# Kernel tuning notes

Hardware: AMD Instinct MI355X
Metric: run time of the kernel (lower is better)

Reference implementation:

```python
import jax, jax.numpy as jnp
import numpy as np

N = 100000
E = 1600000
IN_C = 128
HID = 128
OUT_C = 2
EPS = 1e-5


def gcn_conv(x, src, dst, norm, W, b, num_nodes):
    # PyG GCNConv: linear transform then symmetric-normalized scatter-add
    h = x @ W                                  # [N, out]
    msg = h[src] * norm[:, None]               # [E+N, out] gather
    out = jax.ops.segment_sum(msg, dst, num_segments=num_nodes)
    return out + b


def batchnorm_eval(x, gamma, beta, rm, rv):
    inv = gamma / jnp.sqrt(rv + EPS)
    return (x - rm) * inv + beta


def setup_inputs() -> dict:
    key = jax.random.key(0)
    ks = jax.random.split(key, 16)
    x = jax.random.normal(ks[0], (N, IN_C), dtype=jnp.float32)
    edge_index = jax.random.randint(ks[1], (2, E), 0, N, dtype=jnp.int32)
    s = 1.0 / np.sqrt(IN_C)
    W1 = jax.random.uniform(ks[2], (IN_C, HID), jnp.float32, -s, s)
    b1 = jnp.zeros((HID,), jnp.float32)
    g1 = jnp.ones((HID,), jnp.float32)
    be1 = jnp.zeros((HID,), jnp.float32)
    rm1 = jax.random.normal(ks[3], (HID,), jnp.float32) * 0.1
    rv1 = jax.random.uniform(ks[4], (HID,), jnp.float32, 0.5, 1.5)
    s2 = 1.0 / np.sqrt(HID)
    W2 = jax.random.uniform(ks[5], (HID, HID), jnp.float32, -s2, s2)
    b2 = jnp.zeros((HID,), jnp.float32)
    g2 = jnp.ones((HID,), jnp.float32)
    be2 = jnp.zeros((HID,), jnp.float32)
    rm2 = jax.random.normal(ks[6], (HID,), jnp.float32) * 0.1
    rv2 = jax.random.uniform(ks[7], (HID,), jnp.float32, 0.5, 1.5)
    W3 = jax.random.uniform(ks[8], (HID, OUT_C), jnp.float32, -s2, s2)
    b3 = jnp.zeros((OUT_C,), jnp.float32)
    return {"x": x, "edge_index": edge_index,
            "W1": W1, "b1": b1, "g1": g1, "be1": be1, "rm1": rm1, "rv1": rv1,
            "W2": W2, "b2": b2, "g2": g2, "be2": be2, "rm2": rm2, "rv2": rv2,
            "W3": W3, "b3": b3}


def reference(x, edge_index, W1, b1, g1, be1, rm1, rv1,
              W2, b2, g2, be2, rm2, rv2, W3, b3):
    num_nodes = x.shape[0]
    loops = jnp.arange(num_nodes, dtype=edge_index.dtype)
    src = jnp.concatenate([edge_index[0], loops])   # add self loops
    dst = jnp.concatenate([edge_index[1], loops])
    deg = jax.ops.segment_sum(jnp.ones_like(dst, dtype=x.dtype), dst,
                              num_segments=num_nodes)
    dinv = jax.lax.rsqrt(deg)                        # deg >= 1 with self loops
    norm = dinv[src] * dinv[dst]                     # [E+N]

    h = gcn_conv(x, src, dst, norm, W1, b1, num_nodes)
    h = jax.nn.relu(batchnorm_eval(h, g1, be1, rm1, rv1))
    h = gcn_conv(h, src, dst, norm, W2, b2, num_nodes)
    h = jax.nn.relu(batchnorm_eval(h, g2, be2, rm2, rv2))
    out = gcn_conv(h, src, dst, norm, W3, b3, num_nodes)
    return out
```

## Files before the change

kernel.cpp:

```cpp
#include <hip/hip_runtime.h>

#define NN 100000
#define EE 1600000
#define CH 128

typedef _Float16 h2 __attribute__((ext_vector_type(2)));
typedef _Float16 h8 __attribute__((ext_vector_type(8)));
typedef float f32x4 __attribute__((ext_vector_type(4)));

#define S_NODES 512
#define NBUCK 196
#define CAP_E 10240

#define CHUNK_STRIDE ((size_t)NN * 16)


__global__ __launch_bounds__(256) void k_passA(const int* __restrict__ src, const int* __restrict__ dst,
                                               int* __restrict__ gcur, int* __restrict__ eb) {
    __shared__ int hist[NBUCK];
    __shared__ int curL[NBUCK];
    for (int t = threadIdx.x; t < NBUCK; t += 256) hist[t] = 0;
    __syncthreads();
    int base = blockIdx.x * 4096;
    int pk[16], bk[16];
#pragma unroll
    for (int j = 0; j < 16; ++j) {
        int i = base + threadIdx.x + 256 * j;
        if (i < EE) {
            int s = src[i], d = dst[i];
            bk[j] = d >> 9;
            pk[j] = (s << 9) | (d & 511);
            atomicAdd(&hist[bk[j]], 1);
        } else bk[j] = -1;
    }
    __syncthreads();
    for (int t = threadIdx.x; t < NBUCK; t += 256) {
        int h = hist[t];
        curL[t] = (h > 0) ? atomicAdd(&gcur[t], h) : 0;
    }
    __syncthreads();
#pragma unroll
    for (int j = 0; j < 16; ++j) {
        if (bk[j] >= 0) {
            int pos = atomicAdd(&curL[bk[j]], 1);
            if (pos < CAP_E) eb[bk[j] * CAP_E + pos] = pk[j];
        }
    }
}


__global__ __launch_bounds__(256) void k_bscan(const int* __restrict__ gcur, int* __restrict__ bbase,
                                               int* __restrict__ rp) {
    __shared__ int ts[256];
    int t = threadIdx.x;
    int nn = (t < NBUCK) ? min(S_NODES, NN - t * S_NODES) : 0;
    int v = (t < NBUCK) ? (min(gcur[t], CAP_E) + nn) : 0;
    ts[t] = v; __syncthreads();
    for (int off = 1; off < 256; off <<= 1) {
        int u = (t >= off) ? ts[t - off] : 0;
        __syncthreads();
        ts[t] += u;
        __syncthreads();
    }
    if (t < NBUCK) bbase[t] = ts[t] - v;
    if (t == 0) rp[NN] = EE + NN;
}


__global__ __launch_bounds__(256) void k_passB(const int* __restrict__ gcur, const int* __restrict__ eb,
                                               const int* __restrict__ bbase, int* __restrict__ rp,
                                               float* __restrict__ dinv, int* __restrict__ col) {
    __shared__ int c[S_NODES];
    __shared__ int excl[S_NODES];
    __shared__ int cur[S_NODES];
    __shared__ int ts[256];
    __shared__ int stage[CAP_E + S_NODES];
    int bId = blockIdx.x;
    int nbase = bId * S_NODES;
    int tid = threadIdx.x;
    c[tid] = 0; c[tid + 256] = 0;
    __syncthreads();
    int n = min(gcur[bId], CAP_E);
    const int* e = eb + (size_t)bId * CAP_E;
    for (int i = tid; i < n; i += 256) atomicAdd(&c[e[i] & 511], 1);
    __syncthreads();
    int n0 = nbase + 2 * tid, n1 = n0 + 1;
    int v0 = (n0 < NN) ? c[2 * tid] + 1 : 0;
    int v1 = (n1 < NN) ? c[2 * tid + 1] + 1 : 0;
    int s = v0 + v1;
    ts[tid] = s; __syncthreads();
    for (int off = 1; off < 256; off <<= 1) {
        int u = (tid >= off) ? ts[tid - off] : 0;
        __syncthreads();
        ts[tid] += u;
        __syncthreads();
    }
    int ex = ts[tid] - s;
    int base = bbase[bId];
    excl[2 * tid] = ex; excl[2 * tid + 1] = ex + v0;
    cur[2 * tid] = ex;  cur[2 * tid + 1] = ex + v0;
    if (n0 < NN) { rp[n0] = base + ex;      dinv[n0] = rsqrtf((float)v0); }
    if (n1 < NN) { rp[n1] = base + ex + v0; dinv[n1] = rsqrtf((float)v1); }
    __syncthreads();
    for (int i = tid; i < n; i += 256) {
        int pe = e[i];
        int pos = atomicAdd(&cur[pe & 511], 1);
        stage[pos] = pe >> 9;
    }
    {
        int t0 = 2 * tid, t1 = 2 * tid + 1;
        if (n0 < NN) stage[excl[t0] + c[t0]] = n0;
        if (n1 < NN) stage[excl[t1] + c[t1]] = n1;
    }
    __syncthreads();
    int total = ts[255];
    for (int i = tid; i < total; i += 256) col[base + i] = stage[i];
}


__global__ __launch_bounds__(128) void k_prep(const float* __restrict__ W1, const float* __restrict__ W2,
                                              _Float16* __restrict__ Wt1, _Float16* __restrict__ Wt2,
                                              const float* __restrict__ b1, const float* __restrict__ g1,
                                              const float* __restrict__ be1, const float* __restrict__ rm1,
                                              const float* __restrict__ rv1,
                                              const float* __restrict__ b2, const float* __restrict__ g2,
                                              const float* __restrict__ be2, const float* __restrict__ rm2,
                                              const float* __restrict__ rv2,
                                              float* __restrict__ sc1, float* __restrict__ sh1,
                                              float* __restrict__ sc2, float* __restrict__ sh2) {
    int bid = blockIdx.x, t = threadIdx.x;
    if (bid < 128) {
        Wt1[bid * 128 + t] = (_Float16)W1[t * 128 + bid];
    } else if (bid < 256) {
        int nn = bid - 128;
        Wt2[nn * 128 + t] = (_Float16)W2[t * 128 + nn];
    } else if (bid == 256) {
        float sv = g1[t] * rsqrtf(rv1[t] + 1e-5f);
        sc1[t] = sv;
        sh1[t] = (b1[t] - rm1[t]) * sv + be1[t];
    } else {
        float sv = g2[t] * rsqrtf(rv2[t] + 1e-5f);
        sc2[t] = sv;
        sh2[t] = (b2[t] - rm2[t]) * sv + be2[t];
    }
}


template <bool F32IN>
__global__ __launch_bounds__(256) void k_gemm_mfma(const void* __restrict__ Ain,
                                                   const _Float16* __restrict__ Wt,
                                                   const float* __restrict__ dinv,
                                                   _Float16* __restrict__ C) {
    __shared__ _Float16 Wl[CH * CH];
    {
        const float4* wg = (const float4*)Wt;
#pragma unroll
        for (int i = 0; i < 8; ++i) {
            int chunk = i * 256 + threadIdx.x;
            int row = chunk >> 4, slot = chunk & 15;
            float4 v = wg[chunk];
            *(float4*)((char*)Wl + row * 256 + ((slot ^ (row & 15)) * 16)) = v;
        }
    }
    __syncthreads();
    int lane = threadIdx.x & 63;
    int l15 = lane & 15, lhi = lane >> 4;
    int row0 = blockIdx.x * 64 + (threadIdx.x >> 6) * 16;
    if (row0 >= NN) return;

    h8 afrag[4];
    if (F32IN) {
        const float* Arow = (const float*)Ain + (size_t)(row0 + l15) * CH + lhi * 8;
#pragma unroll
        for (int ks = 0; ks < 4; ++ks) {
            float4 a = *(const float4*)(Arow + ks * 32);
            float4 b = *(const float4*)(Arow + ks * 32 + 4);
            h8 o;
            o[0] = (_Float16)a.x; o[1] = (_Float16)a.y; o[2] = (_Float16)a.z; o[3] = (_Float16)a.w;
            o[4] = (_Float16)b.x; o[5] = (_Float16)b.y; o[6] = (_Float16)b.z; o[7] = (_Float16)b.w;
            afrag[ks] = o;
        }
    } else {
        const _Float16* Ah = (const _Float16*)Ain;
#pragma unroll
        for (int ks = 0; ks < 4; ++ks) {
            int chunk = ks * 2 + (lhi >> 1);
            afrag[ks] = *(const h8*)(Ah + (size_t)chunk * CHUNK_STRIDE
                                     + (size_t)(row0 + l15) * 16 + (lhi & 1) * 8);
        }
    }

    f32x4 acc[8] = {};
#pragma unroll
    for (int ks = 0; ks < 4; ++ks) {
        int slot = ks * 4 + lhi;
#pragma unroll
        for (int c = 0; c < 8; ++c) {
            int brow = c * 16 + l15;
            h8 b = *(const h8*)((char*)Wl + brow * 256 + ((slot ^ (brow & 15)) * 16));
            acc[c] = __builtin_amdgcn_mfma_f32_16x16x32_f16(afrag[ks], b, acc[c], 0, 0, 0);
        }
    }
    float dv[4];
#pragma unroll
    for (int j = 0; j < 4; ++j) dv[j] = dinv[row0 + lhi * 4 + j];
#pragma unroll
    for (int c = 0; c < 8; ++c)
#pragma unroll
        for (int j = 0; j < 4; ++j) {
            float v = acc[c][j] * dv[j];
            C[(size_t)c * CHUNK_STRIDE + (size_t)(row0 + lhi * 4 + j) * 16 + l15] = (_Float16)v;
        }
}


__global__ __launch_bounds__(256) void k_aggs3(const _Float16* __restrict__ h, const int* __restrict__ rp,
                                               const int* __restrict__ col, const float* __restrict__ dinv,
                                               const float* __restrict__ sc, const float* __restrict__ sh,
                                               _Float16* __restrict__ out) {
    int s = blockIdx.x & 7;
    int gb = blockIdx.x >> 3;
    int lane = threadIdx.x & 63;
    int g = lane >> 3;
    int c = lane & 7;
    int node = gb * 32 + (threadIdx.x >> 6) * 8 + g;
    int beg = rp[node];
    int end = rp[node + 1];
    int md = end - beg;
    md = max(md, __shfl_xor(md, 8));
    md = max(md, __shfl_xor(md, 16));
    md = max(md, __shfl_xor(md, 32));
    const _Float16* hs = h + (size_t)s * CHUNK_STRIDE;
    float ax = 0.f, ay = 0.f, bx = 0.f, by = 0.f;
    for (int e = 0; e < md; e += 8) {
        int sv[8]; float m[8];
#pragma unroll
        for (int j = 0; j < 8; ++j) {
            int i = beg + e + j;
            m[j] = (i < end) ? 1.f : 0.f;
            sv[j] = col[i < end ? i : beg];
        }
        h2 v[8];
#pragma unroll
        for (int j = 0; j < 8; ++j)
            v[j] = *(const h2*)(hs + ((size_t)sv[j] << 4) + c * 2);
#pragma unroll
        for (int j = 0; j < 8; j += 2) {
            ax = fmaf((float)v[j][0],     m[j],     ax);
            ay = fmaf((float)v[j][1],     m[j],     ay);
            bx = fmaf((float)v[j + 1][0], m[j + 1], bx);
            by = fmaf((float)v[j + 1][1], m[j + 1], by);
        }
    }
    ax += bx; ay += by;
    float dvn = dinv[node];
    float2 scv = *(const float2*)(sc + s * 16 + c * 2);
    float2 shv = *(const float2*)(sh + s * 16 + c * 2);
    float o0 = fmaxf(fmaf(ax * dvn, scv.x, shv.x), 0.f);
    float o1 = fmaxf(fmaf(ay * dvn, scv.y, shv.y), 0.f);
    h2 o; o[0] = (_Float16)o0; o[1] = (_Float16)o1;
    *(h2*)(out + (size_t)s * CHUNK_STRIDE + (size_t)node * 16 + c * 2) = o;
}


__global__ __launch_bounds__(256) void k_gemm_out(const _Float16* __restrict__ A, const float* __restrict__ W3,
                                                  const float* __restrict__ dinv, float* __restrict__ H3) {
    __shared__ float w3s[256];
    w3s[threadIdx.x] = W3[threadIdx.x];
    __syncthreads();
    int n = blockIdx.x * 256 + threadIdx.x;
    if (n >= NN) return;
    float a0 = 0.f, a1 = 0.f;
#pragma unroll
    for (int c = 0; c < 8; ++c) {
        h8 a = *(const h8*)(A + (size_t)c * CHUNK_STRIDE + (size_t)n * 16);
        h8 b = *(const h8*)(A + (size_t)c * CHUNK_STRIDE + (size_t)n * 16 + 8);
#pragma unroll
        for (int j = 0; j < 8; ++j) {
            int k = c * 16 + j;
            a0 += (float)a[j] * w3s[k * 2];
            a1 += (float)a[j] * w3s[k * 2 + 1];
        }
#pragma unroll
        for (int j = 0; j < 8; ++j) {
            int k = c * 16 + 8 + j;
            a0 += (float)b[j] * w3s[k * 2];
            a1 += (float)b[j] * w3s[k * 2 + 1];
        }
    }
    float dv = dinv[n];
    *(float2*)(H3 + (size_t)n * 2) = make_float2(a0 * dv, a1 * dv);
}

__global__ __launch_bounds__(256) void k_agg_out(const float* __restrict__ H3, const int* __restrict__ rp,
                                                 const int* __restrict__ col, const float* __restrict__ dinv,
                                                 const float* __restrict__ b3, float* __restrict__ out) {
    int n = blockIdx.x * 256 + threadIdx.x;
    if (n >= NN) return;
    int beg = rp[n], end = rp[n + 1];
    float a0 = 0.f, a1 = 0.f;
    for (int e = beg; e < end; ++e) {
        int s = col[e];
        float2 hv = *(const float2*)(H3 + (size_t)s * 2);
        a0 += hv.x;
        a1 += hv.y;
    }
    float dv = dinv[n];
    out[(size_t)n * 2 + 0] = fmaf(a0, dv, b3[0]);
    out[(size_t)n * 2 + 1] = fmaf(a1, dv, b3[1]);
}


extern "C" void kernel_launch(void* const* d_in, const int* in_sizes, int n_in,
                              void* d_out, int out_size, void* d_ws, size_t ws_size,
                              hipStream_t stream) {
    const float* x  = (const float*)d_in[0];
    const int* ei   = (const int*)d_in[1];
    const int* src  = ei;
    const int* dst  = ei + EE;
    const float* W1 = (const float*)d_in[2];
    const float* b1 = (const float*)d_in[3];
    const float* g1 = (const float*)d_in[4];
    const float* be1 = (const float*)d_in[5];
    const float* rm1 = (const float*)d_in[6];
    const float* rv1 = (const float*)d_in[7];
    const float* W2 = (const float*)d_in[8];
    const float* b2 = (const float*)d_in[9];
    const float* g2 = (const float*)d_in[10];
    const float* be2 = (const float*)d_in[11];
    const float* rm2 = (const float*)d_in[12];
    const float* rv2 = (const float*)d_in[13];
    const float* W3 = (const float*)d_in[14];
    const float* b3 = (const float*)d_in[15];
    float* out = (float*)d_out;

    char* p = (char*)d_ws;
    auto carve = [&](size_t bytes) -> void* {
        void* r = (void*)p;
        p += (bytes + 255) & ~(size_t)255;
        return r;
    };
    int* rp     = (int*)carve((size_t)(NN + 1) * 4);
    float* dinv = (float*)carve((size_t)NN * 4);
    int* col    = (int*)carve((size_t)(EE + NN) * 4);
    int* bbase  = (int*)carve(256 * 4);
    float* sc1  = (float*)carve(128 * 4);
    float* sh1  = (float*)carve(128 * 4);
    float* sc2  = (float*)carve(128 * 4);
    float* sh2  = (float*)carve(128 * 4);
    _Float16* bufA = (_Float16*)carve((size_t)NN * CH * 2);
    _Float16* bufB = (_Float16*)carve((size_t)NN * CH * 2);
    _Float16* Wt1  = (_Float16*)carve(128 * 128 * 2);
    _Float16* Wt2  = (_Float16*)carve(128 * 128 * 2);
    float* h3   = (float*)carve((size_t)NN * 2 * 4);

    int* eb   = (int*)bufA;
    int* gcur = eb + (size_t)NBUCK * CAP_E;

    hipMemsetAsync(gcur, 0, (size_t)NBUCK * 4, stream);

    k_passA<<<(EE + 4095) / 4096, 256, 0, stream>>>(src, dst, gcur, eb);
    k_bscan<<<1, 256, 0, stream>>>(gcur, bbase, rp);
    k_passB<<<NBUCK, 256, 0, stream>>>(gcur, eb, bbase, rp, dinv, col);
    k_prep<<<258, 128, 0, stream>>>(W1, W2, Wt1, Wt2,
                                    b1, g1, be1, rm1, rv1,
                                    b2, g2, be2, rm2, rv2,
                                    sc1, sh1, sc2, sh2);

    int aggBlocks = 8 * (NN / 32);
    k_gemm_mfma<true><<<(NN + 63) / 64, 256, 0, stream>>>(x, Wt1, dinv, bufA);
    k_aggs3<<<aggBlocks, 256, 0, stream>>>(bufA, rp, col, dinv, sc1, sh1, bufB);
    k_gemm_mfma<false><<<(NN + 63) / 64, 256, 0, stream>>>(bufB, Wt2, dinv, bufA);
    k_aggs3<<<aggBlocks, 256, 0, stream>>>(bufA, rp, col, dinv, sc2, sh2, bufB);
    k_gemm_out<<<(NN + 255) / 256, 256, 0, stream>>>(bufB, W3, dinv, h3);
    k_agg_out<<<(NN + 255) / 256, 256, 0, stream>>>(h3, rp, col, dinv, b3, out);
}
```

Baseline: 270.0 us.

## Sort nodes by degree and aggregate 32 nodes per wave with 16-byte gathers

Adds a counting sort of nodes by in-degree (histogram, scan, scatter into a permutation), so each wavefront in the hidden-layer aggregation handles 32 nodes of similar degree. The per-wave loop bound, which is the maximum degree in the wave, then stays close to every node's own degree. Each lane now gathers 8 halves (16 bytes) per edge instead of 2, which cuts the number of load instructions. The cost is three extra small kernels, two extra memsets and some padding on the col array, and neighbouring output rows are no longer written together.

```diff
diff --git a/kernel.cpp b/kernel.cpp
--- a/kernel.cpp
+++ b/kernel.cpp
@@ -69,7 +69,8 @@
 
 __global__ __launch_bounds__(256) void k_passB(const int* __restrict__ gcur, const int* __restrict__ eb,
                                                const int* __restrict__ bbase, int* __restrict__ rp,
-                                               float* __restrict__ dinv, int* __restrict__ col) {
+                                               float* __restrict__ dinv, int* __restrict__ col,
+                                               int* __restrict__ deg) {
     __shared__ int c[S_NODES];
     __shared__ int excl[S_NODES];
     __shared__ int cur[S_NODES];
@@ -99,8 +100,8 @@
     int base = bbase[bId];
     excl[2 * tid] = ex; excl[2 * tid + 1] = ex + v0;
     cur[2 * tid] = ex;  cur[2 * tid + 1] = ex + v0;
-    if (n0 < NN) { rp[n0] = base + ex;      dinv[n0] = rsqrtf((float)v0); }
-    if (n1 < NN) { rp[n1] = base + ex + v0; dinv[n1] = rsqrtf((float)v1); }
+    if (n0 < NN) { rp[n0] = base + ex;      dinv[n0] = rsqrtf((float)v0); deg[n0] = v0; }
+    if (n1 < NN) { rp[n1] = base + ex + v0; dinv[n1] = rsqrtf((float)v1); deg[n1] = v1; }
     __syncthreads();
     for (int i = tid; i < n; i += 256) {
         int pe = e[i];
@@ -115,6 +116,51 @@
     __syncthreads();
     int total = ts[255];
     for (int i = tid; i < total; i += 256) col[base + i] = stage[i];
+}
+
+
+__global__ __launch_bounds__(256) void k_dhist(const int* __restrict__ deg, int* __restrict__ ghist) {
+    __shared__ int lh[64];
+    int tid = threadIdx.x;
+    if (tid < 64) lh[tid] = 0;
+    __syncthreads();
+    int node = blockIdx.x * 256 + tid;
+    if (node < NN) atomicAdd(&lh[min(deg[node], 63)], 1);
+    __syncthreads();
+    if (tid < 64 && lh[tid] > 0) atomicAdd(&ghist[tid], lh[tid]);
+}
+
+__global__ __launch_bounds__(64) void k_dscan(const int* __restrict__ ghist, int* __restrict__ gcur) {
+    __shared__ int ts[64];
+    int t = threadIdx.x;
+    int v = ghist[t];
+    ts[t] = v; __syncthreads();
+    for (int off = 1; off < 64; off <<= 1) {
+        int u = (t >= off) ? ts[t - off] : 0;
+        __syncthreads();
+        ts[t] += u;
+        __syncthreads();
+    }
+    gcur[t] = ts[t] - v;
+}
+
+__global__ __launch_bounds__(256) void k_dsort(const int* __restrict__ deg, int* __restrict__ gcur,
+                                               int* __restrict__ perm) {
+    __shared__ int lh[64];
+    __shared__ int lbase[64];
+    int tid = threadIdx.x;
+    if (tid < 64) lh[tid] = 0;
+    __syncthreads();
+    int node = blockIdx.x * 256 + tid;
+    int d = -1, lr = 0;
+    if (node < NN) {
+        d = min(deg[node], 63);
+        lr = atomicAdd(&lh[d], 1);
+    }
+    __syncthreads();
+    if (tid < 64) lbase[tid] = (lh[tid] > 0) ? atomicAdd(&gcur[tid], lh[tid]) : 0;
+    __syncthreads();
+    if (node < NN) perm[lbase[d] + lr] = node;
 }
 
 
@@ -214,52 +260,63 @@
 }
 
 
-__global__ __launch_bounds__(256) void k_aggs3(const _Float16* __restrict__ h, const int* __restrict__ rp,
-                                               const int* __restrict__ col, const float* __restrict__ dinv,
+#define UNROLL 8
+
+__global__ __launch_bounds__(256) void k_aggs4(const _Float16* __restrict__ h, const int* __restrict__ rp,
+                                               const int* __restrict__ col, const int* __restrict__ perm,
+                                               const float* __restrict__ dinv,
                                                const float* __restrict__ sc, const float* __restrict__ sh,
                                                _Float16* __restrict__ out) {
     int s = blockIdx.x & 7;
-    int gb = blockIdx.x >> 3;
+    int gw = (blockIdx.x >> 3) * 4 + (threadIdx.x >> 6);
+    int base = gw * 32;
+    if (base >= NN) return;
     int lane = threadIdx.x & 63;
-    int g = lane >> 3;
-    int c = lane & 7;
-    int node = gb * 32 + (threadIdx.x >> 6) * 8 + g;
-    int beg = rp[node];
-    int end = rp[node + 1];
+    int half = lane & 1;
+    int node = perm[base + (lane >> 1)];
+    int beg = rp[node], end = rp[node + 1];
     int md = end - beg;
+    md = max(md, __shfl_xor(md, 2));
+    md = max(md, __shfl_xor(md, 4));
     md = max(md, __shfl_xor(md, 8));
     md = max(md, __shfl_xor(md, 16));
     md = max(md, __shfl_xor(md, 32));
-    const _Float16* hs = h + (size_t)s * CHUNK_STRIDE;
-    float ax = 0.f, ay = 0.f, bx = 0.f, by = 0.f;
-    for (int e = 0; e < md; e += 8) {
-        int sv[8]; float m[8];
-#pragma unroll
-        for (int j = 0; j < 8; ++j) {
+    const _Float16* hs = h + (size_t)s * CHUNK_STRIDE + half * 8;
+    float acc[8] = {};
+    for (int e = 0; e < md; e += UNROLL) {
+        int idx[UNROLL]; float m[UNROLL];
+#pragma unroll
+        for (int j = 0; j < UNROLL; ++j) {
             int i = beg + e + j;
+            idx[j] = col[i];
             m[j] = (i < end) ? 1.f : 0.f;
-            sv[j] = col[i < end ? i : beg];
-        }
-        h2 v[8];
-#pragma unroll
-        for (int j = 0; j < 8; ++j)
-            v[j] = *(const h2*)(hs + ((size_t)sv[j] << 4) + c * 2);
-#pragma unroll
-        for (int j = 0; j < 8; j += 2) {
-            ax = fmaf((float)v[j][0],     m[j],     ax);
-            ay = fmaf((float)v[j][1],     m[j],     ay);
-            bx = fmaf((float)v[j + 1][0], m[j + 1], bx);
-            by = fmaf((float)v[j + 1][1], m[j + 1], by);
-        }
-    }
-    ax += bx; ay += by;
+        }
+        h8 v[UNROLL];
+#pragma unroll
+        for (int j = 0; j < UNROLL; ++j)
+            v[j] = *(const h8*)(hs + ((size_t)idx[j] << 4));
+#pragma unroll
+        for (int j = 0; j < UNROLL; ++j)
+#pragma unroll
+            for (int k = 0; k < 8; ++k)
+                acc[k] = fmaf((float)v[j][k], m[j], acc[k]);
+    }
     float dvn = dinv[node];
-    float2 scv = *(const float2*)(sc + s * 16 + c * 2);
-    float2 shv = *(const float2*)(sh + s * 16 + c * 2);
-    float o0 = fmaxf(fmaf(ax * dvn, scv.x, shv.x), 0.f);
-    float o1 = fmaxf(fmaf(ay * dvn, scv.y, shv.y), 0.f);
-    h2 o; o[0] = (_Float16)o0; o[1] = (_Float16)o1;
-    *(h2*)(out + (size_t)s * CHUNK_STRIDE + (size_t)node * 16 + c * 2) = o;
+    int cb = s * 16 + half * 8;
+    float4 s0 = *(const float4*)(sc + cb);
+    float4 s1 = *(const float4*)(sc + cb + 4);
+    float4 t0 = *(const float4*)(sh + cb);
+    float4 t1 = *(const float4*)(sh + cb + 4);
+    h8 o;
+    o[0] = (_Float16)fmaxf(fmaf(acc[0] * dvn, s0.x, t0.x), 0.f);
+    o[1] = (_Float16)fmaxf(fmaf(acc[1] * dvn, s0.y, t0.y), 0.f);
+    o[2] = (_Float16)fmaxf(fmaf(acc[2] * dvn, s0.z, t0.z), 0.f);
+    o[3] = (_Float16)fmaxf(fmaf(acc[3] * dvn, s0.w, t0.w), 0.f);
+    o[4] = (_Float16)fmaxf(fmaf(acc[4] * dvn, s1.x, t1.x), 0.f);
+    o[5] = (_Float16)fmaxf(fmaf(acc[5] * dvn, s1.y, t1.y), 0.f);
+    o[6] = (_Float16)fmaxf(fmaf(acc[6] * dvn, s1.z, t1.z), 0.f);
+    o[7] = (_Float16)fmaxf(fmaf(acc[7] * dvn, s1.w, t1.w), 0.f);
+    *(h8*)(out + (size_t)s * CHUNK_STRIDE + (size_t)node * 16 + half * 8) = o;
 }
 
 
@@ -342,8 +399,12 @@
     };
     int* rp     = (int*)carve((size_t)(NN + 1) * 4);
     float* dinv = (float*)carve((size_t)NN * 4);
-    int* col    = (int*)carve((size_t)(EE + NN) * 4);
+    int* col    = (int*)carve((size_t)(EE + NN + 64) * 4);
     int* bbase  = (int*)carve(256 * 4);
+    int* deg    = (int*)carve((size_t)NN * 4);
+    int* perm   = (int*)carve((size_t)NN * 4);
+    int* ghist  = (int*)carve(64 * 4);
+    int* dcur   = (int*)carve(64 * 4);
     float* sc1  = (float*)carve(128 * 4);
     float* sh1  = (float*)carve(128 * 4);
     float* sc2  = (float*)carve(128 * 4);
@@ -358,20 +419,26 @@
     int* gcur = eb + (size_t)NBUCK * CAP_E;
 
     hipMemsetAsync(gcur, 0, (size_t)NBUCK * 4, stream);
-
+    hipMemsetAsync(ghist, 0, 64 * 4, stream);
+    hipMemsetAsync(col + EE + NN, 0, 64 * 4, stream);
+
+    int nblk = (NN + 255) / 256;
     k_passA<<<(EE + 4095) / 4096, 256, 0, stream>>>(src, dst, gcur, eb);
     k_bscan<<<1, 256, 0, stream>>>(gcur, bbase, rp);
-    k_passB<<<NBUCK, 256, 0, stream>>>(gcur, eb, bbase, rp, dinv, col);
+    k_passB<<<NBUCK, 256, 0, stream>>>(gcur, eb, bbase, rp, dinv, col, deg);
+    k_dhist<<<nblk, 256, 0, stream>>>(deg, ghist);
+    k_dscan<<<1, 64, 0, stream>>>(ghist, dcur);
+    k_dsort<<<nblk, 256, 0, stream>>>(deg, dcur, perm);
     k_prep<<<258, 128, 0, stream>>>(W1, W2, Wt1, Wt2,
                                     b1, g1, be1, rm1, rv1,
                                     b2, g2, be2, rm2, rv2,
                                     sc1, sh1, sc2, sh2);
 
-    int aggBlocks = 8 * (NN / 32);
+    int aggBlocks = 8 * ((NN / 32 + 3) / 4);
     k_gemm_mfma<true><<<(NN + 63) / 64, 256, 0, stream>>>(x, Wt1, dinv, bufA);
-    k_aggs3<<<aggBlocks, 256, 0, stream>>>(bufA, rp, col, dinv, sc1, sh1, bufB);
+    k_aggs4<<<aggBlocks, 256, 0, stream>>>(bufA, rp, col, perm, dinv, sc1, sh1, bufB);
     k_gemm_mfma<false><<<(NN + 63) / 64, 256, 0, stream>>>(bufB, Wt2, dinv, bufA);
-    k_aggs3<<<aggBlocks, 256, 0, stream>>>(bufA, rp, col, dinv, sc2, sh2, bufB);
+    k_aggs4<<<aggBlocks, 256, 0, stream>>>(bufA, rp, col, perm, dinv, sc2, sh2, bufB);
     k_gemm_out<<<(NN + 255) / 256, 256, 0, stream>>>(bufB, W3, dinv, h3);
     k_agg_out<<<(NN + 255) / 256, 256, 0, stream>>>(h3, rp, col, dinv, b3, out);
 }
```

Result: slower. 353.3 us (+30.8%).
